# Kernel tuning notes

Hardware: AMD Instinct MI355X
Metric: run time of the kernel (lower is better)

The kernel has to match this reference:

```python
import jax, jax.numpy as jnp
import numpy as np

D = 768      # feature_dim
HD = 768     # hidden_dim
NH = 4       # num_heads
B, T1, T2 = 4, 128, 128
LN_EPS = 1e-5

def setup_inputs() -> dict:
    key = jax.random.key(0)
    ks = jax.random.split(key, 12)
    s = 0.02
    return {
        'speech_features': jax.random.normal(ks[0], (B, T1, D), jnp.float32),
        'phoneme_features': jax.random.normal(ks[1], (B, T2, D), jnp.float32),
        # per-head attention MLP: Linear(2D->HD), ReLU, Linear(HD->1); stacked over heads
        'W1': jax.random.normal(ks[2], (NH, 2 * D, HD), jnp.float32) * s,
        'b1': jnp.zeros((NH, HD), jnp.float32),
        'w2': jax.random.normal(ks[3], (NH, HD), jnp.float32) * s,
        'b2': jnp.zeros((NH,), jnp.float32),
        # fusion: Linear(2D->2HD), ReLU, Linear(2HD->D), LayerNorm(D)
        'Wf1': jax.random.normal(ks[4], (2 * D, 2 * HD), jnp.float32) * s,
        'bf1': jnp.zeros((2 * HD,), jnp.float32),
        'Wf2': jax.random.normal(ks[5], (2 * HD, D), jnp.float32) * s,
        'bf2': jnp.zeros((D,), jnp.float32),
        'ln_g': jnp.ones((D,), jnp.float32),
        'ln_b': jnp.zeros((D,), jnp.float32),
    }

def reference(speech_features, phoneme_features, W1, b1, w2, b2, Wf1, bf1, Wf2, bf2, ln_g, ln_b):
    d = speech_features.shape[-1]
    # Decompose Linear(cat([speech_t, phoneme])) = speech@W1[:d] + phoneme@W1[d:] + b1
    Wx, Wy = W1[:, :d, :], W1[:, d:, :]
    sx = jnp.einsum('btd,ndh->nbth', speech_features, Wx)   # [NH,B,T1,HD]
    py = jnp.einsum('bsd,ndh->nbsh', phoneme_features, Wy)  # [NH,B,T2,HD]
    hidden = jax.nn.relu(sx[:, :, :, None, :] + py[:, :, None, :, :]
                         + b1[:, None, None, None, :])      # [NH,B,T1,T2,HD]
    scores = jnp.einsum('nbtsh,nh->nbts', hidden, w2) + b2[:, None, None, None]
    attn = jax.nn.softmax(scores, axis=-1).mean(axis=0)     # [B,T1,T2]
    context = jnp.einsum('bts,bsd->btd', attn, phoneme_features)  # [B,T1,D]
    fused = jnp.concatenate([speech_features, context], axis=-1)  # [B,T1,2D]
    # dropout is identity in eval mode
    h = jax.nn.relu(fused @ Wf1 + bf1)
    out = h @ Wf2 + bf2
    mu = out.mean(axis=-1, keepdims=True)
    var = ((out - mu) ** 2).mean(axis=-1, keepdims=True)
    out = (out - mu) * jax.lax.rsqrt(var + LN_EPS) * ln_g + ln_b
    return out.mean(axis=1)  # [B,D]
```

## Files before the change

### kernel.cpp

```cpp
#include <hip/hip_runtime.h>
#include <cstddef>


#define D_  768
#define HD_ 768
#define NH_ 4
#define B_  4
#define T1_ 128
#define T2_ 128
#define M_  (B_*T1_)
#define LN_EPS_ 1e-5f

typedef unsigned short u16;
typedef unsigned int u32;
typedef _Float16 f16;
typedef _Float16 f16x2 __attribute__((ext_vector_type(2)));
typedef __bf16 bf16x8 __attribute__((ext_vector_type(8)));
typedef float f32x4 __attribute__((ext_vector_type(4)));

__device__ __forceinline__ u16 f2bf(float f) {
    union { float f; unsigned int u; } v; v.f = f;
    unsigned int u = v.u + (0x7FFFu + ((v.u >> 16) & 1u));
    return (u16)(u >> 16);
}
__device__ __forceinline__ u16 f16bits(f16 h) {
    return __builtin_bit_cast(unsigned short, h);
}
__device__ __forceinline__ u32 splat2(u16 h) {
    return (u32)h * 0x10001u;
}
__device__ __forceinline__ u32 pk_add(u32 a, u32 b) {
    u32 d; asm("v_pk_add_f16 %0, %1, %2" : "=v"(d) : "v"(a), "v"(b)); return d;
}
__device__ __forceinline__ u32 pk_max0(u32 a) {
    u32 d; asm("v_pk_max_f16 %0, %1, %2" : "=v"(d) : "v"(a), "v"(0u)); return d;
}
__device__ __forceinline__ u32 pk_fma(u32 a, u32 b, u32 c) {
    u32 d; asm("v_pk_fma_f16 %0, %1, %2, %3" : "=v"(d) : "v"(a), "v"(b), "v"(c)); return d;
}
__device__ __forceinline__ float lo_f(u32 u) {
    f16x2 v = __builtin_bit_cast(f16x2, u); return (float)v.x;
}
__device__ __forceinline__ float hi_f(u32 u) {
    f16x2 v = __builtin_bit_cast(f16x2, u); return (float)v.y;
}

template<bool RELU, int MODE>
__device__ __forceinline__ void gemm_mfma_body(
    const u16* __restrict__ A, int lda,
    const u16* __restrict__ Bt, int ldb,
    const float* __restrict__ bias,
    void* __restrict__ C, int ldc, int K, int m0, int n0)
{
    __shared__ __align__(16) u16 As[64][40];
    __shared__ __align__(16) u16 Bs[64][40];
    __shared__ u16 Ts[MODE == 3 ? 64 : 1][MODE == 3 ? 68 : 1];

    const int tid = threadIdx.x;
    const int row = tid >> 2;
    const int kq  = (tid & 3) << 3;
    const int lane = tid & 63;
    const int w  = tid >> 6;
    const int wr = (w >> 1) << 5;
    const int wc = (w & 1) << 5;
    const int l16 = lane & 15;
    const int lk8 = (lane >> 4) << 3;
    const int r4  = (lane >> 4) << 2;

    const u16* aptr = A + (size_t)(m0 + row) * lda + kq;
    const u16* bptr = Bt + (size_t)(n0 + row) * ldb + kq;

    f32x4 acc00 = {0.f,0.f,0.f,0.f}, acc01 = {0.f,0.f,0.f,0.f};
    f32x4 acc10 = {0.f,0.f,0.f,0.f}, acc11 = {0.f,0.f,0.f,0.f};

    uint4 a_nxt = *(const uint4*)aptr;
    uint4 b_nxt = *(const uint4*)bptr;

    for (int k0 = 0; k0 < K; k0 += 32) {
        __syncthreads();
        *(uint4*)&As[row][kq] = a_nxt;
        *(uint4*)&Bs[row][kq] = b_nxt;
        if (k0 + 32 < K) {
            a_nxt = *(const uint4*)(aptr + k0 + 32);
            b_nxt = *(const uint4*)(bptr + k0 + 32);
        }
        __syncthreads();
        bf16x8 af0 = *(const bf16x8*)&As[wr + l16][lk8];
        bf16x8 af1 = *(const bf16x8*)&As[wr + 16 + l16][lk8];
        bf16x8 bf0 = *(const bf16x8*)&Bs[wc + l16][lk8];
        bf16x8 bf1 = *(const bf16x8*)&Bs[wc + 16 + l16][lk8];
        acc00 = __builtin_amdgcn_mfma_f32_16x16x32_bf16(af0, bf0, acc00, 0, 0, 0);
        acc01 = __builtin_amdgcn_mfma_f32_16x16x32_bf16(af0, bf1, acc01, 0, 0, 0);
        acc10 = __builtin_amdgcn_mfma_f32_16x16x32_bf16(af1, bf0, acc10, 0, 0, 0);
        acc11 = __builtin_amdgcn_mfma_f32_16x16x32_bf16(af1, bf1, acc11, 0, 0, 0);
    }

#define EPI_FRAG(ACC, MF, NF)                                                  \
    {                                                                          \
        const int gcol = n0 + wc + (NF)*16 + l16;                              \
        const float bv = bias ? bias[gcol] : 0.f;                              \
        float v_[4];                                                           \
        _Pragma("unroll")                                                      \
        for (int r = 0; r < 4; r++) {                                          \
            float v = ACC[r] + bv;                                             \
            if (RELU) v = fmaxf(v, 0.f);                                       \
            v_[r] = v;                                                         \
        }                                                                      \
        const int lr0 = wr + (MF)*16 + r4;                                     \
        if (MODE == 3) {                                                       \
            const int lc = wc + (NF)*16 + l16;                                 \
            _Pragma("unroll")                                                  \
            for (int r = 0; r < 4; r++) Ts[lc][lr0 + r] = f16bits((f16)v_[r]); \
        } else {                                                               \
            _Pragma("unroll")                                                  \
            for (int r = 0; r < 4; r++) {                                      \
                const size_t off = (size_t)(m0 + lr0 + r) * ldc + gcol;        \
                if (MODE == 0) ((float*)C)[off] = v_[r];                       \
                else if (MODE == 1) ((u16*)C)[off] = f2bf(v_[r]);              \
                else ((u16*)C)[off] = f16bits((f16)v_[r]);                     \
            }                                                                  \
        }                                                                      \
    }
    EPI_FRAG(acc00, 0, 0) EPI_FRAG(acc01, 0, 1)
    EPI_FRAG(acc10, 1, 0) EPI_FRAG(acc11, 1, 1)
#undef EPI_FRAG

    if (MODE == 3) {
        __syncthreads();
        u16* cb = (u16*)C + (size_t)(m0 >> 7) * (768 * 128) + (m0 & 127);
#pragma unroll
        for (int u = 0; u < 4; u++) {
            const int i = tid + u * 256;
            const int hl = i >> 4;
            const int s4 = (i & 15) << 2;
            ushort4 o;
            o.x = Ts[hl][s4 + 0]; o.y = Ts[hl][s4 + 1];
            o.z = Ts[hl][s4 + 2]; o.w = Ts[hl][s4 + 3];
            *(ushort4*)(cb + (size_t)(n0 + hl) * 128 + s4) = o;
        }
    }
}

__global__ __launch_bounds__(256) void prep_kernel(
    const float* __restrict__ speech, const float* __restrict__ phon,
    const float* __restrict__ W1, const float* __restrict__ Wf1,
    const float* __restrict__ Wf2,
    u16* __restrict__ spb, u16* __restrict__ phb,
    u16* __restrict__ w1t, u16* __restrict__ wf1t, u16* __restrict__ wf2t)
{
    const int tid = threadIdx.x;
    int bid = blockIdx.x;
    if (bid < 768) {
        const bool isp = bid < 384;
        const float* in = isp ? speech : phon;
        u16* outb = isp ? spb : phb;
        const int i = ((isp ? bid : bid - 384) * 256 + tid) * 4;
        float4 v = *(const float4*)(in + i);
        ushort4 o;
        o.x = f2bf(v.x); o.y = f2bf(v.y); o.z = f2bf(v.z); o.w = f2bf(v.w);
        *(ushort4*)(outb + i) = o;
        return;
    }
    bid -= 768;
    const float* in; u16* outp; int tx, ty;
    if (bid < 4608) {
        const int z = bid / 1152, r = bid % 1152;
        tx = r % 24; ty = r / 24;
        in = W1 + (size_t)z * 1536 * 768; outp = w1t + (size_t)z * 768 * 1536;
    } else if (bid < 6912) {
        const int r = bid - 4608;
        tx = r % 48; ty = r / 48;
        in = Wf1; outp = wf1t;
    } else {
        const int r = bid - 6912;
        tx = r % 24; ty = r / 24;
        in = Wf2; outp = wf2t;
    }
    const int C = (bid >= 4608 && bid < 6912) ? 1536 : 768;
    const int c0 = tx * 32, r0 = ty * 32;
    __shared__ float tile[32][33];
    const int tr = tid >> 3, tc = (tid & 7) << 2;
    float4 v = *(const float4*)(in + (size_t)(r0 + tr) * C + c0 + tc);
    tile[tr][tc] = v.x; tile[tr][tc + 1] = v.y; tile[tr][tc + 2] = v.z; tile[tr][tc + 3] = v.w;
    __syncthreads();
    ushort4 o;
    o.x = f2bf(tile[tc + 0][tr]); o.y = f2bf(tile[tc + 1][tr]);
    o.z = f2bf(tile[tc + 2][tr]); o.w = f2bf(tile[tc + 3][tr]);
    *(ushort4*)(outp + (size_t)(c0 + tr) * 1536 + r0 + tc) = o;
}

__global__ __launch_bounds__(256) void gemm_sxpy_kernel(
    const u16* __restrict__ sp, const u16* __restrict__ ph,
    const u16* __restrict__ w1t, const float* __restrict__ b1,
    u16* __restrict__ sxf, u16* __restrict__ pyt)
{
    const int z = blockIdx.z;
    const int n = z & 3;
    const bool ispy = z >= 4;
    const u16* Bt = w1t + (size_t)n * 768 * 1536 + (ispy ? 768 : 0);
    if (!ispy) {
        gemm_mfma_body<false, 2>(sp, 768, Bt, 1536, b1 + n * HD_,
                                 sxf + (size_t)n * M_ * HD_, HD_, 768,
                                 blockIdx.y * 64, blockIdx.x * 64);
    } else {
        gemm_mfma_body<false, 3>(ph, 768, Bt, 1536, nullptr,
                                 pyt + (size_t)n * 4 * 768 * 128, 0, 768,
                                 blockIdx.y * 64, blockIdx.x * 64);
    }
}

template<bool RELU, int MODE>
__global__ __launch_bounds__(256) void gemm_mfma_kernel(
    const u16* __restrict__ A, int lda,
    const u16* __restrict__ Bt, int ldb,
    const float* __restrict__ bias,
    void* __restrict__ C, int ldc, int K)
{
    gemm_mfma_body<RELU, MODE>(A, lda, Bt, ldb, bias, C, ldc, K,
                               blockIdx.y * 64, blockIdx.x * 64);
}

__global__ __launch_bounds__(256) void scores_softmax_kernel(
    const u16* __restrict__ sxf,
    const u16* __restrict__ pyt,
    const float* __restrict__ w2,
    float* __restrict__ probs)
{
    const int bid = blockIdx.x;
    const int n = bid >> 6, b = (bid >> 4) & 3, t0 = (bid & 15) * 8;
    const int tid = threadIdx.x, lane = tid & 63, w = tid >> 6;

    __shared__ __align__(16) u32 sxs[8][768];
    __shared__ __align__(16) u32 w2s[768];

    for (int q = 0; q < 6; q++) {
        const int u = tid + q * 256;
        const int r = u / 192;
        const int h4 = (u % 192) * 4;
        ushort4 v = *(const ushort4*)(sxf + ((size_t)(n * 512 + b * 128 + t0 + r)) * 768 + h4);
        sxs[r][h4 + 0] = splat2(v.x);
        sxs[r][h4 + 1] = splat2(v.y);
        sxs[r][h4 + 2] = splat2(v.z);
        sxs[r][h4 + 3] = splat2(v.w);
    }
    for (int q = 0; q < 3; q++) {
        const int i = tid + q * 256;
        w2s[i] = splat2(f16bits((f16)w2[n * 768 + i]));
    }
    __syncthreads();

    const u32* pypanel = (const u32*)(pyt + ((size_t)((n << 2) | b)) * 768 * 128) + lane;

    float accA0 = 0.f, accA1 = 0.f, accB0 = 0.f, accB1 = 0.f;
    const int rA = 2 * w, rB = 2 * w + 1;

    u32 b0[16], b1[16];
#pragma unroll
    for (int j = 0; j < 16; j++) b0[j] = pypanel[(size_t)j * 64];
#pragma unroll
    for (int j = 0; j < 16; j++) b1[j] = pypanel[(size_t)(16 + j) * 64];

    auto compute = [&](const u32 (&buf)[16], int hbase) {
        u32 aA = 0u, aB = 0u;
#pragma unroll
        for (int j = 0; j < 16; j++) {
            const u32 p = buf[j];
            const u32 wj = w2s[hbase + j];
            aA = pk_fma(pk_max0(pk_add(sxs[rA][hbase + j], p)), wj, aA);
            aB = pk_fma(pk_max0(pk_add(sxs[rB][hbase + j], p)), wj, aB);
        }
        accA0 += lo_f(aA); accA1 += hi_f(aA);
        accB0 += lo_f(aB); accB1 += hi_f(aB);
    };

    for (int hc = 0; hc < 768; hc += 32) {
        compute(b0, hc);
        if (hc + 32 < 768) {
#pragma unroll
            for (int j = 0; j < 16; j++) b0[j] = pypanel[(size_t)(hc + 32 + j) * 64];
        }
        compute(b1, hc + 16);
        if (hc + 48 < 768) {
#pragma unroll
            for (int j = 0; j < 16; j++) b1[j] = pypanel[(size_t)(hc + 48 + j) * 64];
        }
    }

#pragma unroll
    for (int which = 0; which < 2; which++) {
        const float s0 = which ? accB0 : accA0;
        const float s1 = which ? accB1 : accA1;
        const int t = t0 + 2 * w + which;
        float mx = fmaxf(s0, s1);
#pragma unroll
        for (int off = 32; off; off >>= 1) mx = fmaxf(mx, __shfl_xor(mx, off, 64));
        const float e0 = expf(s0 - mx), e1 = expf(s1 - mx);
        float sm = e0 + e1;
#pragma unroll
        for (int off = 32; off; off >>= 1) sm += __shfl_xor(sm, off, 64);
        const float inv = 0.25f / sm;
        float2 pr; pr.x = e0 * inv; pr.y = e1 * inv;
        *(float2*)&probs[((size_t)(n * 512 + b * 128 + t)) * 128 + 2 * lane] = pr;
    }
}

__global__ __launch_bounds__(256) void context_fused_kernel(
    const float* __restrict__ probs, const float* __restrict__ phon,
    const float* __restrict__ speech, u16* __restrict__ fused)
{
    const int m = blockIdx.x;
    const int b = m >> 7;
    const int tid = threadIdx.x;
    __shared__ float attn[T2_];
    if (tid < T2_) {
        float a = 0.f;
#pragma unroll
        for (int n = 0; n < NH_; n++)
            a += probs[(size_t)(n * M_ + m) * T2_ + tid];
        attn[tid] = a;
    }
    __syncthreads();
    const float* ph = phon + (size_t)b * T2_ * D_;
#pragma unroll
    for (int j = 0; j < 3; j++) {
        const int d = tid + 256 * j;
        float acc = 0.f;
#pragma unroll 8
        for (int s = 0; s < T2_; s++)
            acc = fmaf(attn[s], ph[(size_t)s * D_ + d], acc);
        fused[(size_t)m * (2 * D_) + d] = f2bf(speech[(size_t)m * D_ + d]);
        fused[(size_t)m * (2 * D_) + D_ + d] = f2bf(acc);
    }
}

__global__ __launch_bounds__(256) void ln_fused_kernel(
    const float* __restrict__ x, const float* __restrict__ g,
    const float* __restrict__ lb, float* __restrict__ out)
{
    const int b = blockIdx.x, tid = threadIdx.x, lane = tid & 63, w = tid >> 6;
    __shared__ float rs[T1_];
    __shared__ float Sred[4];

    float prsum = 0.f;
    for (int i = 0; i < 32; i++) {
        const int row = w * 32 + i;
        const float4* x4 = (const float4*)(x + ((size_t)(b * T1_ + row)) * D_);
        float s = 0.f, ss = 0.f;
#pragma unroll
        for (int j = 0; j < 3; j++) {
            float4 v = x4[j * 64 + lane];
            s += v.x + v.y + v.z + v.w;
            ss += v.x * v.x + v.y * v.y + v.z * v.z + v.w * v.w;
        }
#pragma unroll
        for (int off = 32; off; off >>= 1) {
            s += __shfl_xor(s, off, 64);
            ss += __shfl_xor(ss, off, 64);
        }
        if (lane == 0) {
            const float mu = s * (1.f / D_);
            const float var = ss * (1.f / D_) - mu * mu;
            const float r = rsqrtf(var + LN_EPS_);
            rs[row] = r;
            prsum += mu * r;
        }
    }
    if (lane == 0) Sred[w] = prsum;
    __syncthreads();
    const float S = Sred[0] + Sred[1] + Sred[2] + Sred[3];
    const float* xb = x + (size_t)b * T1_ * D_;
#pragma unroll
    for (int j = 0; j < 3; j++) {
        const int d = tid + 256 * j;
        float acc = 0.f;
#pragma unroll 8
        for (int t = 0; t < T1_; t++)
            acc = fmaf(xb[(size_t)t * D_ + d], rs[t], acc);
        out[b * D_ + d] = g[d] * (acc - S) * (1.f / T1_) + lb[d];
    }
}

extern "C" void kernel_launch(void* const* d_in, const int* in_sizes, int n_in,
                              void* d_out, int out_size, void* d_ws, size_t ws_size,
                              hipStream_t stream)
{
    const float* speech = (const float*)d_in[0];
    const float* phon   = (const float*)d_in[1];
    const float* W1     = (const float*)d_in[2];
    const float* b1     = (const float*)d_in[3];
    const float* w2     = (const float*)d_in[4];
    const float* Wf1    = (const float*)d_in[6];
    const float* bf1    = (const float*)d_in[7];
    const float* Wf2    = (const float*)d_in[8];
    const float* bf2    = (const float*)d_in[9];
    const float* ln_g   = (const float*)d_in[10];
    const float* ln_b   = (const float*)d_in[11];
    float* out = (float*)d_out;

    char* w = (char*)d_ws;
    auto alloc = [&](size_t bytes) { char* p = w; w += (bytes + 1023) & ~(size_t)1023; return p; };
    u16* sp_bf  = (u16*)alloc((size_t)M_ * D_ * 2);
    u16* ph_bf  = (u16*)alloc((size_t)M_ * D_ * 2);
    u16* w1t    = (u16*)alloc((size_t)NH_ * 768 * 1536 * 2);
    u16* wf1t   = (u16*)alloc((size_t)1536 * 1536 * 2);
    u16* wf2t   = (u16*)alloc((size_t)768 * 1536 * 2);
    u16* sxf    = (u16*)alloc((size_t)NH_ * M_ * HD_ * 2);
    u16* pyt    = (u16*)alloc((size_t)NH_ * B_ * 768 * 128 * 2);
    float* probs  = (float*)alloc((size_t)NH_ * M_ * T2_ * 4);
    u16* fusedb = (u16*)alloc((size_t)M_ * 2 * D_ * 2);
    u16* hbuf   = (u16*)alloc((size_t)M_ * 2 * HD_ * 2);
    float* outpre = (float*)alloc((size_t)M_ * D_ * 4);

    hipLaunchKernelGGL(prep_kernel, dim3(8832), dim3(256), 0, stream,
                       speech, phon, W1, Wf1, Wf2, sp_bf, ph_bf, w1t, wf1t, wf2t);
    hipLaunchKernelGGL(gemm_sxpy_kernel, dim3(HD_ / 64, M_ / 64, 8), dim3(256), 0, stream,
                       sp_bf, ph_bf, w1t, b1, sxf, pyt);
    hipLaunchKernelGGL(scores_softmax_kernel, dim3(256), dim3(256), 0, stream,
                       sxf, pyt, w2, probs);
    hipLaunchKernelGGL(context_fused_kernel, dim3(M_), dim3(256), 0, stream,
                       probs, phon, speech, fusedb);
    hipLaunchKernelGGL((gemm_mfma_kernel<true, 1>), dim3(2 * HD_ / 64, M_ / 64), dim3(256), 0, stream,
                       fusedb, 2 * D_, wf1t, 1536, bf1, hbuf, 2 * HD_, 2 * D_);
    hipLaunchKernelGGL((gemm_mfma_kernel<false, 0>), dim3(D_ / 64, M_ / 64), dim3(256), 0, stream,
                       hbuf, 2 * HD_, wf2t, 1536, bf2, outpre, D_, 2 * HD_);
    hipLaunchKernelGGL(ln_fused_kernel, dim3(B_), dim3(256), 0, stream,
                       outpre, ln_g, ln_b, out);
}
```

Baseline: 141.6 us.

## Merge pipeline into cooperative persistent megakernel with fused fp32-to-bf16 conversion

Replaces the seven separate launches with one cooperative persistent kernel that runs each stage as a phase separated by grid-wide syncs, falling back to per-phase launches if the cooperative launch fails. The separate prep pass that converted and transposed inputs and weights to bf16 is removed. GEMM tiles now load fp32 directly and truncate to bf16 while staging into shared memory. The LayerNorm-mean stage is split into a parallel row-stats phase and a small reduction phase. This aims to cut launch gaps and the prep traffic, at the cost of grid-sync overhead, bf16 truncation instead of rounding, and fp32 intermediate buffers.

```diff
diff --git a/kernel.cpp b/kernel.cpp
--- a/kernel.cpp
+++ b/kernel.cpp
@@ -1,9 +1,11 @@
 #include <hip/hip_runtime.h>
+#include <hip/hip_cooperative_groups.h>
 #include <cstddef>
 
+namespace cg = cooperative_groups;
+
 
 #define D_  768
-#define HD_ 768
 #define NH_ 4
 #define B_  4
 #define T1_ 128
@@ -18,72 +20,73 @@
 typedef __bf16 bf16x8 __attribute__((ext_vector_type(8)));
 typedef float f32x4 __attribute__((ext_vector_type(4)));
 
-__device__ __forceinline__ u16 f2bf(float f) {
-    union { float f; unsigned int u; } v; v.f = f;
-    unsigned int u = v.u + (0x7FFFu + ((v.u >> 16) & 1u));
-    return (u16)(u >> 16);
-}
 __device__ __forceinline__ u16 f16bits(f16 h) {
     return __builtin_bit_cast(unsigned short, h);
 }
-__device__ __forceinline__ u32 splat2(u16 h) {
-    return (u32)h * 0x10001u;
-}
-__device__ __forceinline__ u32 pk_add(u32 a, u32 b) {
-    u32 d; asm("v_pk_add_f16 %0, %1, %2" : "=v"(d) : "v"(a), "v"(b)); return d;
-}
-__device__ __forceinline__ u32 pk_max0(u32 a) {
-    u32 d; asm("v_pk_max_f16 %0, %1, %2" : "=v"(d) : "v"(a), "v"(0u)); return d;
-}
-__device__ __forceinline__ u32 pk_fma(u32 a, u32 b, u32 c) {
-    u32 d; asm("v_pk_fma_f16 %0, %1, %2, %3" : "=v"(d) : "v"(a), "v"(b), "v"(c)); return d;
-}
-__device__ __forceinline__ float lo_f(u32 u) {
-    f16x2 v = __builtin_bit_cast(f16x2, u); return (float)v.x;
-}
-__device__ __forceinline__ float hi_f(u32 u) {
-    f16x2 v = __builtin_bit_cast(f16x2, u); return (float)v.y;
-}
-
-template<bool RELU, int MODE>
-__device__ __forceinline__ void gemm_mfma_body(
-    const u16* __restrict__ A, int lda,
-    const u16* __restrict__ Bt, int ldb,
-    const float* __restrict__ bias,
-    void* __restrict__ C, int ldc, int K, int m0, int n0)
-{
-    __shared__ __align__(16) u16 As[64][40];
-    __shared__ __align__(16) u16 Bs[64][40];
-    __shared__ u16 Ts[MODE == 3 ? 64 : 1][MODE == 3 ? 68 : 1];
-
-    const int tid = threadIdx.x;
+__device__ __forceinline__ f16x2 bcast2(u32 u) {
+    return __builtin_bit_cast(f16x2, u);
+}
+__device__ __forceinline__ u32 splat2(u16 h) { return (u32)h * 0x10001u; }
+__device__ __forceinline__ u32 pack_trunc(float lo, float hi) {
+    u32 a = __builtin_bit_cast(u32, lo), b = __builtin_bit_cast(u32, hi);
+    return (b & 0xFFFF0000u) | (a >> 16);
+}
+
+struct Params {
+    const float *speech, *phon, *W1, *b1, *w2, *Wf1, *bf1, *Wf2, *bf2, *g, *lb;
+    float* out;
+    u16 *sxf, *pyt;
+    float *probs, *ctx, *hbuf, *outpre, *rs, *prS;
+};
+
+#define SMEM_BYTES 28672
+
+template<int MODE, bool RELU, bool SPLIT>
+__device__ __forceinline__ void gemm_tile(
+    const float* __restrict__ A1, const float* __restrict__ A2, int lda,
+    const float* __restrict__ B, int ldb,
+    const float* __restrict__ bias, void* __restrict__ C, int ldc,
+    int K, int m0, int n0, char* smem, int tid)
+{
+    u16 (*As)[40] = reinterpret_cast<u16(*)[40]>(smem);
+    u16 (*Bs)[40] = reinterpret_cast<u16(*)[40]>(smem + 5120);
+    u16 (*Ts)[68] = reinterpret_cast<u16(*)[68]>(smem + 10240);
+
     const int row = tid >> 2;
     const int kq  = (tid & 3) << 3;
-    const int lane = tid & 63;
-    const int w  = tid >> 6;
-    const int wr = (w >> 1) << 5;
-    const int wc = (w & 1) << 5;
-    const int l16 = lane & 15;
-    const int lk8 = (lane >> 4) << 3;
-    const int r4  = (lane >> 4) << 2;
-
-    const u16* aptr = A + (size_t)(m0 + row) * lda + kq;
-    const u16* bptr = Bt + (size_t)(n0 + row) * ldb + kq;
+    const int kp  = tid >> 4;
+    const int nq  = (tid & 15) << 2;
+    const int lane = tid & 63, w = tid >> 6;
+    const int wr = (w >> 1) << 5, wc = (w & 1) << 5;
+    const int l16 = lane & 15, lk8 = (lane >> 4) << 3, r4 = (lane >> 4) << 2;
 
     f32x4 acc00 = {0.f,0.f,0.f,0.f}, acc01 = {0.f,0.f,0.f,0.f};
     f32x4 acc10 = {0.f,0.f,0.f,0.f}, acc11 = {0.f,0.f,0.f,0.f};
 
-    uint4 a_nxt = *(const uint4*)aptr;
-    uint4 b_nxt = *(const uint4*)bptr;
+    float4 ax, ay, bx, by;
+    auto loadA = [&](int k0) {
+        const float* src = A1; int kk = k0;
+        if (SPLIT && k0 >= 768) { src = A2; kk = k0 - 768; }
+        const float* ap = src + (size_t)(m0 + row) * lda + kk + kq;
+        ax = *(const float4*)ap; ay = *(const float4*)(ap + 4);
+    };
+    auto loadB = [&](int k0) {
+        const float* bp = B + (size_t)(k0 + 2 * kp) * ldb + n0 + nq;
+        bx = *(const float4*)bp; by = *(const float4*)(bp + ldb);
+    };
+    loadA(0); loadB(0);
 
     for (int k0 = 0; k0 < K; k0 += 32) {
         __syncthreads();
-        *(uint4*)&As[row][kq] = a_nxt;
-        *(uint4*)&Bs[row][kq] = b_nxt;
-        if (k0 + 32 < K) {
-            a_nxt = *(const uint4*)(aptr + k0 + 32);
-            b_nxt = *(const uint4*)(bptr + k0 + 32);
-        }
+        uint4 apk;
+        apk.x = pack_trunc(ax.x, ax.y); apk.y = pack_trunc(ax.z, ax.w);
+        apk.z = pack_trunc(ay.x, ay.y); apk.w = pack_trunc(ay.z, ay.w);
+        *(uint4*)&As[row][kq] = apk;
+        *(u32*)&Bs[nq + 0][2 * kp] = pack_trunc(bx.x, by.x);
+        *(u32*)&Bs[nq + 1][2 * kp] = pack_trunc(bx.y, by.y);
+        *(u32*)&Bs[nq + 2][2 * kp] = pack_trunc(bx.z, by.z);
+        *(u32*)&Bs[nq + 3][2 * kp] = pack_trunc(bx.w, by.w);
+        if (k0 + 32 < K) { loadA(k0 + 32); loadB(k0 + 32); }
         __syncthreads();
         bf16x8 af0 = *(const bf16x8*)&As[wr + l16][lk8];
         bf16x8 af1 = *(const bf16x8*)&As[wr + 16 + l16][lk8];
@@ -116,7 +119,6 @@
             for (int r = 0; r < 4; r++) {                                      \
                 const size_t off = (size_t)(m0 + lr0 + r) * ldc + gcol;        \
                 if (MODE == 0) ((float*)C)[off] = v_[r];                       \
-                else if (MODE == 1) ((u16*)C)[off] = f2bf(v_[r]);              \
                 else ((u16*)C)[off] = f16bits((f16)v_[r]);                     \
             }                                                                  \
         }                                                                      \
@@ -141,210 +143,175 @@
     }
 }
 
-__global__ __launch_bounds__(256) void prep_kernel(
-    const float* __restrict__ speech, const float* __restrict__ phon,
-    const float* __restrict__ W1, const float* __restrict__ Wf1,
-    const float* __restrict__ Wf2,
-    u16* __restrict__ spb, u16* __restrict__ phb,
-    u16* __restrict__ w1t, u16* __restrict__ wf1t, u16* __restrict__ wf2t)
-{
-    const int tid = threadIdx.x;
-    int bid = blockIdx.x;
-    if (bid < 768) {
-        const bool isp = bid < 384;
-        const float* in = isp ? speech : phon;
-        u16* outb = isp ? spb : phb;
-        const int i = ((isp ? bid : bid - 384) * 256 + tid) * 4;
-        float4 v = *(const float4*)(in + i);
-        ushort4 o;
-        o.x = f2bf(v.x); o.y = f2bf(v.y); o.z = f2bf(v.z); o.w = f2bf(v.w);
-        *(ushort4*)(outb + i) = o;
-        return;
-    }
-    bid -= 768;
-    const float* in; u16* outp; int tx, ty;
-    if (bid < 4608) {
-        const int z = bid / 1152, r = bid % 1152;
-        tx = r % 24; ty = r / 24;
-        in = W1 + (size_t)z * 1536 * 768; outp = w1t + (size_t)z * 768 * 1536;
-    } else if (bid < 6912) {
-        const int r = bid - 4608;
-        tx = r % 48; ty = r / 48;
-        in = Wf1; outp = wf1t;
-    } else {
-        const int r = bid - 6912;
-        tx = r % 24; ty = r / 24;
-        in = Wf2; outp = wf2t;
-    }
-    const int C = (bid >= 4608 && bid < 6912) ? 1536 : 768;
-    const int c0 = tx * 32, r0 = ty * 32;
-    __shared__ float tile[32][33];
-    const int tr = tid >> 3, tc = (tid & 7) << 2;
-    float4 v = *(const float4*)(in + (size_t)(r0 + tr) * C + c0 + tc);
-    tile[tr][tc] = v.x; tile[tr][tc + 1] = v.y; tile[tr][tc + 2] = v.z; tile[tr][tc + 3] = v.w;
-    __syncthreads();
-    ushort4 o;
-    o.x = f2bf(tile[tc + 0][tr]); o.y = f2bf(tile[tc + 1][tr]);
-    o.z = f2bf(tile[tc + 2][tr]); o.w = f2bf(tile[tc + 3][tr]);
-    *(ushort4*)(outp + (size_t)(c0 + tr) * 1536 + r0 + tc) = o;
-}
-
-__global__ __launch_bounds__(256) void gemm_sxpy_kernel(
-    const u16* __restrict__ sp, const u16* __restrict__ ph,
-    const u16* __restrict__ w1t, const float* __restrict__ b1,
-    u16* __restrict__ sxf, u16* __restrict__ pyt)
-{
-    const int z = blockIdx.z;
-    const int n = z & 3;
-    const bool ispy = z >= 4;
-    const u16* Bt = w1t + (size_t)n * 768 * 1536 + (ispy ? 768 : 0);
-    if (!ispy) {
-        gemm_mfma_body<false, 2>(sp, 768, Bt, 1536, b1 + n * HD_,
-                                 sxf + (size_t)n * M_ * HD_, HD_, 768,
-                                 blockIdx.y * 64, blockIdx.x * 64);
-    } else {
-        gemm_mfma_body<false, 3>(ph, 768, Bt, 1536, nullptr,
-                                 pyt + (size_t)n * 4 * 768 * 128, 0, 768,
-                                 blockIdx.y * 64, blockIdx.x * 64);
-    }
-}
-
-template<bool RELU, int MODE>
-__global__ __launch_bounds__(256) void gemm_mfma_kernel(
-    const u16* __restrict__ A, int lda,
-    const u16* __restrict__ Bt, int ldb,
-    const float* __restrict__ bias,
-    void* __restrict__ C, int ldc, int K)
-{
-    gemm_mfma_body<RELU, MODE>(A, lda, Bt, ldb, bias, C, ldc, K,
-                               blockIdx.y * 64, blockIdx.x * 64);
-}
-
-__global__ __launch_bounds__(256) void scores_softmax_kernel(
-    const u16* __restrict__ sxf,
-    const u16* __restrict__ pyt,
-    const float* __restrict__ w2,
-    float* __restrict__ probs)
-{
-    const int bid = blockIdx.x;
-    const int n = bid >> 6, b = (bid >> 4) & 3, t0 = (bid & 15) * 8;
-    const int tid = threadIdx.x, lane = tid & 63, w = tid >> 6;
-
-    __shared__ __align__(16) u32 sxs[8][768];
-    __shared__ __align__(16) u32 w2s[768];
-
-    for (int q = 0; q < 6; q++) {
-        const int u = tid + q * 256;
-        const int r = u / 192;
-        const int h4 = (u % 192) * 4;
-        ushort4 v = *(const ushort4*)(sxf + ((size_t)(n * 512 + b * 128 + t0 + r)) * 768 + h4);
-        sxs[r][h4 + 0] = splat2(v.x);
-        sxs[r][h4 + 1] = splat2(v.y);
-        sxs[r][h4 + 2] = splat2(v.z);
-        sxs[r][h4 + 3] = splat2(v.w);
-    }
-    for (int q = 0; q < 3; q++) {
-        const int i = tid + q * 256;
-        w2s[i] = splat2(f16bits((f16)w2[n * 768 + i]));
-    }
-    __syncthreads();
-
-    const u32* pypanel = (const u32*)(pyt + ((size_t)((n << 2) | b)) * 768 * 128) + lane;
-
-    float accA0 = 0.f, accA1 = 0.f, accB0 = 0.f, accB1 = 0.f;
-    const int rA = 2 * w, rB = 2 * w + 1;
-
-    u32 b0[16], b1[16];
-#pragma unroll
-    for (int j = 0; j < 16; j++) b0[j] = pypanel[(size_t)j * 64];
-#pragma unroll
-    for (int j = 0; j < 16; j++) b1[j] = pypanel[(size_t)(16 + j) * 64];
-
-    auto compute = [&](const u32 (&buf)[16], int hbase) {
-        u32 aA = 0u, aB = 0u;
-#pragma unroll
-        for (int j = 0; j < 16; j++) {
-            const u32 p = buf[j];
-            const u32 wj = w2s[hbase + j];
-            aA = pk_fma(pk_max0(pk_add(sxs[rA][hbase + j], p)), wj, aA);
-            aB = pk_fma(pk_max0(pk_add(sxs[rB][hbase + j], p)), wj, aB);
-        }
-        accA0 += lo_f(aA); accA1 += hi_f(aA);
-        accB0 += lo_f(aB); accB1 += hi_f(aB);
-    };
-
-    for (int hc = 0; hc < 768; hc += 32) {
-        compute(b0, hc);
-        if (hc + 32 < 768) {
-#pragma unroll
-            for (int j = 0; j < 16; j++) b0[j] = pypanel[(size_t)(hc + 32 + j) * 64];
-        }
-        compute(b1, hc + 16);
-        if (hc + 48 < 768) {
-#pragma unroll
-            for (int j = 0; j < 16; j++) b1[j] = pypanel[(size_t)(hc + 48 + j) * 64];
-        }
-    }
-
-#pragma unroll
-    for (int which = 0; which < 2; which++) {
-        const float s0 = which ? accB0 : accA0;
-        const float s1 = which ? accB1 : accA1;
-        const int t = t0 + 2 * w + which;
-        float mx = fmaxf(s0, s1);
-#pragma unroll
-        for (int off = 32; off; off >>= 1) mx = fmaxf(mx, __shfl_xor(mx, off, 64));
-        const float e0 = expf(s0 - mx), e1 = expf(s1 - mx);
-        float sm = e0 + e1;
-#pragma unroll
-        for (int off = 32; off; off >>= 1) sm += __shfl_xor(sm, off, 64);
-        const float inv = 0.25f / sm;
-        float2 pr; pr.x = e0 * inv; pr.y = e1 * inv;
-        *(float2*)&probs[((size_t)(n * 512 + b * 128 + t)) * 128 + 2 * lane] = pr;
-    }
-}
-
-__global__ __launch_bounds__(256) void context_fused_kernel(
-    const float* __restrict__ probs, const float* __restrict__ phon,
-    const float* __restrict__ speech, u16* __restrict__ fused)
-{
-    const int m = blockIdx.x;
-    const int b = m >> 7;
-    const int tid = threadIdx.x;
-    __shared__ float attn[T2_];
-    if (tid < T2_) {
-        float a = 0.f;
-#pragma unroll
-        for (int n = 0; n < NH_; n++)
-            a += probs[(size_t)(n * M_ + m) * T2_ + tid];
-        attn[tid] = a;
-    }
-    __syncthreads();
-    const float* ph = phon + (size_t)b * T2_ * D_;
-#pragma unroll
-    for (int j = 0; j < 3; j++) {
-        const int d = tid + 256 * j;
-        float acc = 0.f;
+__device__ __forceinline__ void phase1(const Params& p, char* smem, int tid,
+                                       unsigned bid, unsigned stride)
+{
+    for (unsigned job = bid; job < 768; job += stride) {
+        const int z = job / 96, r = job % 96, my = r / 12, nx = r % 12;
+        const int n = z & 3;
+        if (z < 4)
+            gemm_tile<2, false, false>(p.speech, nullptr, 768,
+                p.W1 + (size_t)n * 1536 * 768, 768, p.b1 + n * 768,
+                p.sxf + (size_t)n * 512 * 768, 768, 768, my * 64, nx * 64, smem, tid);
+        else
+            gemm_tile<3, false, false>(p.phon, nullptr, 768,
+                p.W1 + (size_t)n * 1536 * 768 + 768 * 768, 768, nullptr,
+                p.pyt + (size_t)n * 4 * 768 * 128, 0, 768, my * 64, nx * 64, smem, tid);
+    }
+}
+
+__device__ __forceinline__ void phase2(const Params& p, char* smem, int tid,
+                                       unsigned bid, unsigned stride)
+{
+    const int lane = tid & 63, w = tid >> 6;
+    for (unsigned job = bid; job < 256; job += stride) {
+        const int n = job >> 6, b = (job >> 4) & 3, t0 = (job & 15) * 8;
+        f16x2 (*sxs)[768] = reinterpret_cast<f16x2(*)[768]>(smem);
+        f16x2* w2s = reinterpret_cast<f16x2*>(smem + 24576);
+
+        __syncthreads();
+        for (int q = 0; q < 6; q++) {
+            const int u = tid + q * 256;
+            const int r = u / 192;
+            const int h4 = (u % 192) * 4;
+            ushort4 v = *(const ushort4*)(p.sxf + ((size_t)(n * 512 + b * 128 + t0 + r)) * 768 + h4);
+            sxs[r][h4 + 0] = bcast2(splat2(v.x));
+            sxs[r][h4 + 1] = bcast2(splat2(v.y));
+            sxs[r][h4 + 2] = bcast2(splat2(v.z));
+            sxs[r][h4 + 3] = bcast2(splat2(v.w));
+        }
+        for (int q = 0; q < 3; q++) {
+            const int i = tid + q * 256;
+            w2s[i] = bcast2(splat2(f16bits((f16)p.w2[n * 768 + i])));
+        }
+        __syncthreads();
+
+        const f16x2* pypanel = (const f16x2*)(p.pyt + ((size_t)((n << 2) | b)) * 768 * 128) + lane;
+        const f16x2 z2 = {(f16)0, (f16)0};
+
+        float accA0 = 0.f, accA1 = 0.f, accB0 = 0.f, accB1 = 0.f;
+        const int rA = 2 * w, rB = 2 * w + 1;
+
+        f16x2 b0[16], b1[16];
+#pragma unroll
+        for (int j = 0; j < 16; j++) b0[j] = pypanel[(size_t)j * 64];
+#pragma unroll
+        for (int j = 0; j < 16; j++) b1[j] = pypanel[(size_t)(16 + j) * 64];
+
+        auto compute = [&](const f16x2 (&buf)[16], int hbase) {
+            f16x2 aA = z2, aB = z2;
+#pragma unroll
+            for (int j4 = 0; j4 < 16; j4 += 4) {
+                uint4 sau = *(const uint4*)&sxs[rA][hbase + j4];
+                uint4 sbu = *(const uint4*)&sxs[rB][hbase + j4];
+                uint4 wvu = *(const uint4*)&w2s[hbase + j4];
+                const u32 sa_[4] = {sau.x, sau.y, sau.z, sau.w};
+                const u32 sb_[4] = {sbu.x, sbu.y, sbu.z, sbu.w};
+                const u32 wv_[4] = {wvu.x, wvu.y, wvu.z, wvu.w};
+#pragma unroll
+                for (int j = 0; j < 4; j++) {
+                    const f16x2 pv = buf[j4 + j];
+                    const f16x2 wj = bcast2(wv_[j]);
+                    f16x2 ra = __builtin_elementwise_max(bcast2(sa_[j]) + pv, z2);
+                    f16x2 rb = __builtin_elementwise_max(bcast2(sb_[j]) + pv, z2);
+                    aA = __builtin_elementwise_fma(ra, wj, aA);
+                    aB = __builtin_elementwise_fma(rb, wj, aB);
+                }
+            }
+            accA0 += (float)aA.x; accA1 += (float)aA.y;
+            accB0 += (float)aB.x; accB1 += (float)aB.y;
+        };
+
+        for (int hc = 0; hc < 768; hc += 32) {
+            compute(b0, hc);
+            if (hc + 32 < 768) {
+#pragma unroll
+                for (int j = 0; j < 16; j++) b0[j] = pypanel[(size_t)(hc + 32 + j) * 64];
+            }
+            compute(b1, hc + 16);
+            if (hc + 48 < 768) {
+#pragma unroll
+                for (int j = 0; j < 16; j++) b1[j] = pypanel[(size_t)(hc + 48 + j) * 64];
+            }
+        }
+
+#pragma unroll
+        for (int which = 0; which < 2; which++) {
+            const float s0 = which ? accB0 : accA0;
+            const float s1 = which ? accB1 : accA1;
+            const int t = t0 + 2 * w + which;
+            float mx = fmaxf(s0, s1);
+#pragma unroll
+            for (int off = 32; off; off >>= 1) mx = fmaxf(mx, __shfl_xor(mx, off, 64));
+            const float e0 = expf(s0 - mx), e1 = expf(s1 - mx);
+            float sm = e0 + e1;
+#pragma unroll
+            for (int off = 32; off; off >>= 1) sm += __shfl_xor(sm, off, 64);
+            const float inv = 0.25f / sm;
+            float2 pr; pr.x = e0 * inv; pr.y = e1 * inv;
+            *(float2*)&p.probs[((size_t)(n * 512 + b * 128 + t)) * 128 + 2 * lane] = pr;
+        }
+    }
+}
+
+__device__ __forceinline__ void phase3(const Params& p, char* smem, int tid,
+                                       unsigned bid, unsigned stride)
+{
+    for (unsigned job = bid; job < 512; job += stride) {
+        const int m = job, b = m >> 7;
+        float* attn = reinterpret_cast<float*>(smem);
+        __syncthreads();
+        if (tid < 128) {
+            float a = 0.f;
+#pragma unroll
+            for (int n = 0; n < 4; n++)
+                a += p.probs[((size_t)(n * 512) + m) * 128 + tid];
+            attn[tid] = a;
+        }
+        __syncthreads();
+        const float* ph = p.phon + (size_t)b * 128 * 768;
+#pragma unroll
+        for (int j = 0; j < 3; j++) {
+            const int d = tid + 256 * j;
+            float acc = 0.f;
 #pragma unroll 8
-        for (int s = 0; s < T2_; s++)
-            acc = fmaf(attn[s], ph[(size_t)s * D_ + d], acc);
-        fused[(size_t)m * (2 * D_) + d] = f2bf(speech[(size_t)m * D_ + d]);
-        fused[(size_t)m * (2 * D_) + D_ + d] = f2bf(acc);
-    }
-}
-
-__global__ __launch_bounds__(256) void ln_fused_kernel(
-    const float* __restrict__ x, const float* __restrict__ g,
-    const float* __restrict__ lb, float* __restrict__ out)
-{
-    const int b = blockIdx.x, tid = threadIdx.x, lane = tid & 63, w = tid >> 6;
-    __shared__ float rs[T1_];
-    __shared__ float Sred[4];
-
-    float prsum = 0.f;
-    for (int i = 0; i < 32; i++) {
-        const int row = w * 32 + i;
-        const float4* x4 = (const float4*)(x + ((size_t)(b * T1_ + row)) * D_);
+            for (int s = 0; s < 128; s++)
+                acc = fmaf(attn[s], ph[(size_t)s * 768 + d], acc);
+            p.ctx[(size_t)m * 768 + d] = acc;
+        }
+    }
+}
+
+__device__ __forceinline__ void phase4(const Params& p, char* smem, int tid,
+                                       unsigned bid, unsigned stride)
+{
+    for (unsigned job = bid; job < 192; job += stride) {
+        const int my = job / 24, nx = job % 24;
+        gemm_tile<0, true, true>(p.speech, p.ctx, 768, p.Wf1, 1536, p.bf1,
+                                 p.hbuf, 1536, 1536, my * 64, nx * 64, smem, tid);
+    }
+}
+
+__device__ __forceinline__ void phase5(const Params& p, char* smem, int tid,
+                                       unsigned bid, unsigned stride)
+{
+    for (unsigned job = bid; job < 96; job += stride) {
+        const int my = job / 12, nx = job % 12;
+        gemm_tile<0, false, false>(p.hbuf, nullptr, 1536, p.Wf2, 768, p.bf2,
+                                   p.outpre, 768, 1536, my * 64, nx * 64, smem, tid);
+    }
+}
+
+__device__ __forceinline__ void phase6(const Params& p, char* smem, int tid,
+                                       unsigned bid, unsigned stride)
+{
+    const int lane = tid & 63, w = tid >> 6;
+    for (unsigned job = bid; job < 128; job += stride) {
+        const int b = job >> 5, q = job & 31;
+        const int rowg = b * 128 + q * 4 + w;
+        float* Sred = reinterpret_cast<float*>(smem);
+        __syncthreads();
+        const float4* x4 = (const float4*)(p.outpre + (size_t)rowg * 768);
         float s = 0.f, ss = 0.f;
 #pragma unroll
         for (int j = 0; j < 3; j++) {
@@ -358,71 +325,115 @@
             ss += __shfl_xor(ss, off, 64);
         }
         if (lane == 0) {
-            const float mu = s * (1.f / D_);
-            const float var = ss * (1.f / D_) - mu * mu;
+            const float mu = s * (1.f / 768.f);
+            const float var = ss * (1.f / 768.f) - mu * mu;
             const float r = rsqrtf(var + LN_EPS_);
-            rs[row] = r;
-            prsum += mu * r;
-        }
-    }
-    if (lane == 0) Sred[w] = prsum;
-    __syncthreads();
-    const float S = Sred[0] + Sred[1] + Sred[2] + Sred[3];
-    const float* xb = x + (size_t)b * T1_ * D_;
-#pragma unroll
-    for (int j = 0; j < 3; j++) {
-        const int d = tid + 256 * j;
+            p.rs[rowg] = r;
+            Sred[w] = mu * r;
+        }
+        __syncthreads();
+        if (tid == 0) p.prS[job] = Sred[0] + Sred[1] + Sred[2] + Sred[3];
+    }
+}
+
+__device__ __forceinline__ void phase7(const Params& p, char* smem, int tid,
+                                       unsigned bid, unsigned stride)
+{
+    for (unsigned job = bid; job < 12; job += stride) {
+        const int b = job / 3, c = job % 3, d = c * 256 + tid;
+        float* rsl = reinterpret_cast<float*>(smem);
+        float* prl = rsl + 128;
+        __syncthreads();
+        if (tid < 128) rsl[tid] = p.rs[b * 128 + tid];
+        else if (tid < 160) prl[tid - 128] = p.prS[b * 32 + (tid - 128)];
+        __syncthreads();
+        float S = 0.f;
+#pragma unroll
+        for (int i = 0; i < 32; i++) S += prl[i];
         float acc = 0.f;
 #pragma unroll 8
-        for (int t = 0; t < T1_; t++)
-            acc = fmaf(xb[(size_t)t * D_ + d], rs[t], acc);
-        out[b * D_ + d] = g[d] * (acc - S) * (1.f / T1_) + lb[d];
-    }
+        for (int t = 0; t < 128; t++)
+            acc = fmaf(p.outpre[(size_t)(b * 128 + t) * 768 + d], rsl[t], acc);
+        p.out[b * 768 + d] = p.g[d] * (acc - S) * (1.f / 128.f) + p.lb[d];
+    }
+}
+
+__global__ __launch_bounds__(256, 2) void mega_kernel(Params p)
+{
+    __shared__ __align__(16) char smem[SMEM_BYTES];
+    const int tid = threadIdx.x;
+    cg::grid_group grid = cg::this_grid();
+    const unsigned bid = blockIdx.x, stride = gridDim.x;
+
+    phase1(p, smem, tid, bid, stride); grid.sync();
+    phase2(p, smem, tid, bid, stride); grid.sync();
+    phase3(p, smem, tid, bid, stride); grid.sync();
+    phase4(p, smem, tid, bid, stride); grid.sync();
+    phase5(p, smem, tid, bid, stride); grid.sync();
+    phase6(p, smem, tid, bid, stride); grid.sync();
+    phase7(p, smem, tid, bid, stride);
+}
+
+template<int PH>
+__global__ __launch_bounds__(256) void phase_kernel(Params p)
+{
+    __shared__ __align__(16) char smem[SMEM_BYTES];
+    const int tid = threadIdx.x;
+    const unsigned bid = blockIdx.x, stride = gridDim.x;
+    if      (PH == 1) phase1(p, smem, tid, bid, stride);
+    else if (PH == 2) phase2(p, smem, tid, bid, stride);
+    else if (PH == 3) phase3(p, smem, tid, bid, stride);
+    else if (PH == 4) phase4(p, smem, tid, bid, stride);
+    else if (PH == 5) phase5(p, smem, tid, bid, stride);
+    else if (PH == 6) phase6(p, smem, tid, bid, stride);
+    else              phase7(p, smem, tid, bid, stride);
 }
 
 extern "C" void kernel_launch(void* const* d_in, const int* in_sizes, int n_in,
                               void* d_out, int out_size, void* d_ws, size_t ws_size,
                               hipStream_t stream)
 {
-    const float* speech = (const float*)d_in[0];
-    const float* phon   = (const float*)d_in[1];
-    const float* W1     = (const float*)d_in[2];
-    const float* b1     = (const float*)d_in[3];
-    const float* w2     = (const float*)d_in[4];
-    const float* Wf1    = (const float*)d_in[6];
-    const float* bf1    = (const float*)d_in[7];
-    const float* Wf2    = (const float*)d_in[8];
-    const float* bf2    = (const float*)d_in[9];
-    const float* ln_g   = (const float*)d_in[10];
-    const float* ln_b   = (const float*)d_in[11];
-    float* out = (float*)d_out;
+    Params p;
+    p.speech = (const float*)d_in[0];
+    p.phon   = (const float*)d_in[1];
+    p.W1     = (const float*)d_in[2];
+    p.b1     = (const float*)d_in[3];
+    p.w2     = (const float*)d_in[4];
+    p.Wf1    = (const float*)d_in[6];
+    p.bf1    = (const float*)d_in[7];
+    p.Wf2    = (const float*)d_in[8];
+    p.bf2    = (const float*)d_in[9];
+    p.g      = (const float*)d_in[10];
+    p.lb     = (const float*)d_in[11];
+    p.out    = (float*)d_out;
 
     char* w = (char*)d_ws;
-    auto alloc = [&](size_t bytes) { char* p = w; w += (bytes + 1023) & ~(size_t)1023; return p; };
-    u16* sp_bf  = (u16*)alloc((size_t)M_ * D_ * 2);
-    u16* ph_bf  = (u16*)alloc((size_t)M_ * D_ * 2);
-    u16* w1t    = (u16*)alloc((size_t)NH_ * 768 * 1536 * 2);
-    u16* wf1t   = (u16*)alloc((size_t)1536 * 1536 * 2);
-    u16* wf2t   = (u16*)alloc((size_t)768 * 1536 * 2);
-    u16* sxf    = (u16*)alloc((size_t)NH_ * M_ * HD_ * 2);
-    u16* pyt    = (u16*)alloc((size_t)NH_ * B_ * 768 * 128 * 2);
-    float* probs  = (float*)alloc((size_t)NH_ * M_ * T2_ * 4);
-    u16* fusedb = (u16*)alloc((size_t)M_ * 2 * D_ * 2);
-    u16* hbuf   = (u16*)alloc((size_t)M_ * 2 * HD_ * 2);
-    float* outpre = (float*)alloc((size_t)M_ * D_ * 4);
-
-    hipLaunchKernelGGL(prep_kernel, dim3(8832), dim3(256), 0, stream,
-                       speech, phon, W1, Wf1, Wf2, sp_bf, ph_bf, w1t, wf1t, wf2t);
-    hipLaunchKernelGGL(gemm_sxpy_kernel, dim3(HD_ / 64, M_ / 64, 8), dim3(256), 0, stream,
-                       sp_bf, ph_bf, w1t, b1, sxf, pyt);
-    hipLaunchKernelGGL(scores_softmax_kernel, dim3(256), dim3(256), 0, stream,
-                       sxf, pyt, w2, probs);
-    hipLaunchKernelGGL(context_fused_kernel, dim3(M_), dim3(256), 0, stream,
-                       probs, phon, speech, fusedb);
-    hipLaunchKernelGGL((gemm_mfma_kernel<true, 1>), dim3(2 * HD_ / 64, M_ / 64), dim3(256), 0, stream,
-                       fusedb, 2 * D_, wf1t, 1536, bf1, hbuf, 2 * HD_, 2 * D_);
-    hipLaunchKernelGGL((gemm_mfma_kernel<false, 0>), dim3(D_ / 64, M_ / 64), dim3(256), 0, stream,
-                       hbuf, 2 * HD_, wf2t, 1536, bf2, outpre, D_, 2 * HD_);
-    hipLaunchKernelGGL(ln_fused_kernel, dim3(B_), dim3(256), 0, stream,
-                       outpre, ln_g, ln_b, out);
-}
+    auto alloc = [&](size_t bytes) { char* q = w; w += (bytes + 1023) & ~(size_t)1023; return q; };
+    p.sxf    = (u16*)alloc((size_t)NH_ * M_ * 768 * 2);
+    p.pyt    = (u16*)alloc((size_t)NH_ * B_ * 768 * 128 * 2);
+    p.probs  = (float*)alloc((size_t)NH_ * M_ * 128 * 4);
+    p.ctx    = (float*)alloc((size_t)M_ * 768 * 4);
+    p.hbuf   = (float*)alloc((size_t)M_ * 1536 * 4);
+    p.outpre = (float*)alloc((size_t)M_ * 768 * 4);
+    p.rs     = (float*)alloc(M_ * 4);
+    p.prS    = (float*)alloc(128 * 4);
+
+    int occ = 0;
+    hipError_t qerr = hipOccupancyMaxActiveBlocksPerMultiprocessor(&occ, mega_kernel, 256, 0);
+    hipError_t lerr = hipErrorUnknown;
+    if (qerr == hipSuccess && occ >= 1) {
+        const unsigned gb = (occ >= 2 ? 2u : 1u) * 256u;
+        void* kargs[] = { (void*)&p };
+        lerr = hipLaunchCooperativeKernel(reinterpret_cast<void*>(mega_kernel),
+                                          dim3(gb), dim3(256), kargs, 0, stream);
+    }
+    if (lerr != hipSuccess) {
+        hipLaunchKernelGGL(phase_kernel<1>, dim3(768), dim3(256), 0, stream, p);
+        hipLaunchKernelGGL(phase_kernel<2>, dim3(256), dim3(256), 0, stream, p);
+        hipLaunchKernelGGL(phase_kernel<3>, dim3(512), dim3(256), 0, stream, p);
+        hipLaunchKernelGGL(phase_kernel<4>, dim3(192), dim3(256), 0, stream, p);
+        hipLaunchKernelGGL(phase_kernel<5>, dim3(96),  dim3(256), 0, stream, p);
+        hipLaunchKernelGGL(phase_kernel<6>, dim3(128), dim3(256), 0, stream, p);
+        hipLaunchKernelGGL(phase_kernel<7>, dim3(12),  dim3(256), 0, stream, p);
+    }
+}
```

Measured after the change: 333.3 us. +135.4%, slower.
